# Kernel optimization log

Measured on AMD Instinct MI355X. Metric: run time of the kernel, lower is better.

Reference implementation:

```python
import jax, jax.numpy as jnp
import numpy as np

TEMPERATURE = 10.0
N_CLASSES = 10


def _sqdist(a, b):
    # squared euclidean distances, [Na, Nb] == torch.cdist(a, b) ** 2
    an = jnp.sum(a * a, axis=1)[:, None]
    bn = jnp.sum(b * b, axis=1)[None, :]
    return jnp.maximum(an + bn - 2.0 * (a @ b.T), 0.0)


def setup_inputs() -> dict:
    key = jax.random.key(0)
    ks = jax.random.split(key, 6)
    B, N, D, H, C = 512, 4096, 512, 2048, N_CLASSES
    return {
        "x": jax.random.normal(ks[0], (B, D), dtype=jnp.float32),
        "star_features": jax.random.normal(ks[1], (N, D), dtype=jnp.float32),
        "from_features": jax.random.normal(ks[2], (N, D), dtype=jnp.float32),
        "star_label_ids": jax.random.randint(ks[3], (N,), 0, C),
        "W1": jax.random.normal(ks[4], (D, H), dtype=jnp.float32) * 0.02,
        "b1": jnp.zeros((H,), dtype=jnp.float32),
        "W2": jax.random.normal(ks[5], (H, C), dtype=jnp.float32) * 0.02,
        "b2": jnp.zeros((C,), dtype=jnp.float32),
    }


def _transport_features(x, feats_to, star_feats):
    # dists: [N_star, B]
    d = _sqdist(star_feats, x)
    d = d / jnp.mean(d, axis=0, keepdims=True)
    e = jnp.exp(-TEMPERATURE * d)                    # [N_star, B]
    w = feats_to.T @ e                               # [d_to, B]
    return (w / jnp.sum(e, axis=0, keepdims=True)).T  # [B, d_to]


def reference(x, star_features, from_features, star_label_ids, W1, b1, W2, b2):
    B = x.shape[0]
    C = N_CLASSES
    # --- exact-match lookup against dataset_star features (fused eq+all reduce) ---
    mask = jnp.all(x[:, None, :] == star_features[None, :, :], axis=2)  # [B, N_star]
    matched = jnp.any(mask, axis=1)                                      # [B]
    match_idx = jnp.argmax(mask, axis=1)                                 # [B]
    # --- transport features: matched samples take aligned dataset sample, rest use OT map ---
    xt_unmatched = _transport_features(x, from_features, star_features)  # [B, d]
    xt_matched = from_features[match_idx]                                # [B, d]
    x_transported = jnp.where(matched[:, None], xt_matched, xt_unmatched)
    # --- run the model in the transported domain (MLP classifier) ---
    h = jax.nn.relu(x_transported @ W1 + b1)
    logits = h @ W2 + b2                                                 # [B, C]
    # --- project_labels: preds and one-hot unique labels have equal dim -> cdist/argmin branch ---
    unique_labels = jnp.eye(C, dtype=logits.dtype)
    closest = jnp.argmin(_sqdist(logits, unique_labels), axis=1)
    y_proj = unique_labels[closest]                                      # [B, C] (unused by 'all_features')
    # --- transport_labels, method='all_features': feature-distance-weighted average of star labels ---
    d2 = _sqdist(from_features, x_transported)                           # [N_from, B]
    d2 = d2 / jnp.mean(d2, axis=0, keepdims=True)
    e2 = jnp.exp(-TEMPERATURE * d2)
    star_labels = jax.nn.one_hot(star_label_ids, C, dtype=x.dtype)       # [N_star, C]
    y_star = (star_labels.T @ e2 / jnp.sum(e2, axis=0, keepdims=True)).T  # [B, C]
    # single (model, dataset) pair -> sum/len is identity
    return y_star
```

## Files before the change

### kernel.cpp

```cpp
#include <hip/hip_runtime.h>

#define TEMP 10.0f
#define NS 4096
#define BB 512
#define DDIM 512
#define NCLS 10

typedef short bf16x8 __attribute__((ext_vector_type(8)));
typedef float f32x4 __attribute__((ext_vector_type(4)));

__device__ inline short f2bf(float f) {
    unsigned u = __builtin_bit_cast(unsigned, f);
    u += 0x7FFFu + ((u >> 16) & 1u);
    return (short)(u >> 16);
}
__device__ inline float bf2f(short h) {
    unsigned u = ((unsigned)(unsigned short)h) << 16;
    return __builtin_bit_cast(float, u);
}

__global__ void init_midx(int* midx) {
    int t = blockIdx.x * 256 + threadIdx.x;
    if (t < BB) midx[t] = NS;
}

__global__ __launch_bounds__(256)
void conv512(const float* __restrict__ in, short* __restrict__ outb,
             float* __restrict__ n2) {
    int row = blockIdx.x * 4 + (threadIdx.x >> 6);
    int l = threadIdx.x & 63;
    const float4* p = (const float4*)(in + (size_t)row * DDIM) + l * 2;
    float4 a = p[0], b = p[1];
    float s = a.x*a.x + a.y*a.y + a.z*a.z + a.w*a.w
            + b.x*b.x + b.y*b.y + b.z*b.z + b.w*b.w;
    bf16x8 h;
    h[0]=f2bf(a.x); h[1]=f2bf(a.y); h[2]=f2bf(a.z); h[3]=f2bf(a.w);
    h[4]=f2bf(b.x); h[5]=f2bf(b.y); h[6]=f2bf(b.z); h[7]=f2bf(b.w);
    *(bf16x8*)(outb + (size_t)row * DDIM + l * 8) = h;
    #pragma unroll
    for (int off = 32; off > 0; off >>= 1) s += __shfl_down(s, off);
    if (l == 0) n2[row] = s;
}

__global__ __launch_bounds__(256)
void convT(const float* __restrict__ in, short* __restrict__ outb) {
    __shared__ short tile[64][72];
    int n0 = blockIdx.x * 64, d0 = blockIdx.y * 64;
    int t = threadIdx.x;
    int r = t >> 4, c4 = (t & 15) * 4;
    #pragma unroll
    for (int rr = 0; rr < 64; rr += 16) {
        float4 v = *(const float4*)(in + (size_t)(n0 + r + rr) * DDIM + d0 + c4);
        tile[r + rr][c4 + 0] = f2bf(v.x);
        tile[r + rr][c4 + 1] = f2bf(v.y);
        tile[r + rr][c4 + 2] = f2bf(v.z);
        tile[r + rr][c4 + 3] = f2bf(v.w);
    }
    __syncthreads();
    int dr = t >> 2, nco = (t & 3) * 16;
    short tmp[16];
    #pragma unroll
    for (int q = 0; q < 16; ++q) tmp[q] = tile[nco + q][dr];
    short* op = outb + (size_t)(d0 + dr) * NS + n0 + nco;
    *(bf16x8*)op       = *(bf16x8*)tmp;
    *(bf16x8*)(op + 8) = *(bf16x8*)(tmp + 8);
}

__global__ void match_kernel(const float* __restrict__ x, const float* __restrict__ star,
                             int* __restrict__ midx) {
    int i = blockIdx.x * blockDim.x + threadIdx.x;
    if (i >= NS * BB) return;
    int b = i & (BB - 1);
    int n = i >> 9;
    const float* xr = x + (size_t)b * DDIM;
    const float* sr = star + (size_t)n * DDIM;
    if (xr[0] != sr[0]) return;
    for (int k = 1; k < DDIM; ++k) if (xr[k] != sr[k]) return;
    atomicMin(&midx[b], n);
}

#define BM 64
#define BN 128
#define BK 64
#define LDSP 72
template<int MODE>
__global__ __launch_bounds__(256)
void gemm_bt(const short* __restrict__ A, const short* __restrict__ B, int K,
             int kslab, int nt, const float* __restrict__ an2,
             const float* __restrict__ bn2, float* __restrict__ C, int ldc,
             size_t cstride) {
    __shared__ short As[2][BM][LDSP];
    __shared__ short Bs[2][BN][LDSP];
    int t = threadIdx.x;
    int m0 = blockIdx.x * BM;
    int n0 = blockIdx.y * BN;
    int kbase = blockIdx.z * kslab;
    float* Cp = C + (size_t)blockIdx.z * cstride;
    int wid = t >> 6, lane = t & 63;
    int wr = wid >> 1, wc = wid & 1;
    int lr = lane & 15, lk = lane >> 4;

    int ar = t >> 2, ak = (t & 3) * 16;
    int br = t >> 1, bk = (t & 1) * 32;
    const short* Ag = A + (size_t)(m0 + ar) * K + kbase + ak;
    const short* Bg = B + (size_t)(n0 + br) * K + kbase + bk;

    f32x4 acc[2][4] = {};
    bf16x8 ra0 = *(const bf16x8*)Ag;
    bf16x8 ra1 = *(const bf16x8*)(Ag + 8);
    bf16x8 rb0 = *(const bf16x8*)Bg;
    bf16x8 rb1 = *(const bf16x8*)(Bg + 8);
    bf16x8 rb2 = *(const bf16x8*)(Bg + 16);
    bf16x8 rb3 = *(const bf16x8*)(Bg + 24);
    int cur = 0;
    *(bf16x8*)&As[0][ar][ak]      = ra0;
    *(bf16x8*)&As[0][ar][ak + 8]  = ra1;
    *(bf16x8*)&Bs[0][br][bk]      = rb0;
    *(bf16x8*)&Bs[0][br][bk + 8]  = rb1;
    *(bf16x8*)&Bs[0][br][bk + 16] = rb2;
    *(bf16x8*)&Bs[0][br][bk + 24] = rb3;

    for (int it = 0; it < nt; ++it) {
        __syncthreads();
        if (it + 1 < nt) {
            int ko = (it + 1) * BK;
            ra0 = *(const bf16x8*)(Ag + ko);
            ra1 = *(const bf16x8*)(Ag + ko + 8);
            rb0 = *(const bf16x8*)(Bg + ko);
            rb1 = *(const bf16x8*)(Bg + ko + 8);
            rb2 = *(const bf16x8*)(Bg + ko + 16);
            rb3 = *(const bf16x8*)(Bg + ko + 24);
        }
        #pragma unroll
        for (int ks = 0; ks < 2; ++ks) {
            int k0 = ks * 32 + lk * 8;
            bf16x8 af[2], bfr[4];
            #pragma unroll
            for (int i = 0; i < 2; ++i)
                af[i] = *(const bf16x8*)&As[cur][wr * 32 + i * 16 + lr][k0];
            #pragma unroll
            for (int j = 0; j < 4; ++j)
                bfr[j] = *(const bf16x8*)&Bs[cur][wc * 64 + j * 16 + lr][k0];
            #pragma unroll
            for (int i = 0; i < 2; ++i)
                #pragma unroll
                for (int j = 0; j < 4; ++j)
                    acc[i][j] = __builtin_amdgcn_mfma_f32_16x16x32_bf16(
                        af[i], bfr[j], acc[i][j], 0, 0, 0);
        }
        if (it + 1 < nt) {
            cur ^= 1;
            *(bf16x8*)&As[cur][ar][ak]      = ra0;
            *(bf16x8*)&As[cur][ar][ak + 8]  = ra1;
            *(bf16x8*)&Bs[cur][br][bk]      = rb0;
            *(bf16x8*)&Bs[cur][br][bk + 8]  = rb1;
            *(bf16x8*)&Bs[cur][br][bk + 16] = rb2;
            *(bf16x8*)&Bs[cur][br][bk + 24] = rb3;
        }
    }
    #pragma unroll
    for (int i = 0; i < 2; ++i) {
        #pragma unroll
        for (int r = 0; r < 4; ++r) {
            int gm = m0 + wr * 32 + i * 16 + lk * 4 + r;
            float a2 = (MODE == 1) ? an2[gm] : 0.0f;
            #pragma unroll
            for (int j = 0; j < 4; ++j) {
                int gn = n0 + wc * 64 + j * 16 + lr;
                float v = acc[i][j][r];
                if (MODE == 1) v = fmaxf(a2 + bn2[gn] - 2.0f * v, 0.0f);
                Cp[(size_t)gm * ldc + gn] = v;
            }
        }
    }
}

__device__ inline float block_sum(float s, float* red) {
    #pragma unroll
    for (int off = 32; off > 0; off >>= 1) s += __shfl_down(s, off);
    int wid = threadIdx.x >> 6;
    if ((threadIdx.x & 63) == 0) red[wid] = s;
    __syncthreads();
    float tot = red[0] + red[1] + red[2] + red[3];
    __syncthreads();
    return tot;
}

__global__ __launch_bounds__(256)
void exp_rows(const float* __restrict__ dT, short* __restrict__ eT,
              float* __restrict__ sumE) {
    __shared__ float red[4];
    int b = blockIdx.x;
    int t = threadIdx.x;
    const float* row = dT + (size_t)b * NS;
    float4 v[4];
    float s = 0.f;
    #pragma unroll
    for (int q = 0; q < 4; ++q) {
        v[q] = *(const float4*)(row + t * 16 + q * 4);
        s += v[q].x + v[q].y + v[q].z + v[q].w;
    }
    float tot = block_sum(s, red);
    float scale = -TEMP * (float)NS / tot;
    float se = 0.f;
    bf16x8 h0, h1;
    #pragma unroll
    for (int q = 0; q < 4; ++q) {
        #pragma unroll
        for (int e = 0; e < 4; ++e) {
            float ev = __expf(v[q][e] * scale);
            short hh = f2bf(ev);
            se += bf2f(hh);
            if (q < 2) h0[q * 4 + e] = hh; else h1[(q - 2) * 4 + e] = hh;
        }
    }
    short* op = eT + (size_t)b * NS + t * 16;
    *(bf16x8*)op       = h0;
    *(bf16x8*)(op + 8) = h1;
    float setot = block_sum(se, red);
    if (t == 0) sumE[b] = setot;
}

__global__ __launch_bounds__(256)
void xt_fin(const float* __restrict__ wpart, const float* __restrict__ sumE,
            const int* __restrict__ midx, const float* __restrict__ fromf,
            short* __restrict__ xtb, float* __restrict__ xtn2) {
    __shared__ float red[4];
    int b = blockIdx.x;
    int t = threadIdx.x;
    int d = t * 2;
    int mi = midx[b];
    float inv = 1.0f / sumE[b];
    float v0 = 0.f, v1 = 0.f;
    #pragma unroll
    for (int sl = 0; sl < 8; ++sl) {
        float2 p = *(const float2*)(wpart + (size_t)sl * (BB * DDIM) + (size_t)b * DDIM + d);
        v0 += p.x; v1 += p.y;
    }
    v0 *= inv; v1 *= inv;
    if (mi < NS) {
        v0 = fromf[(size_t)mi * DDIM + d];
        v1 = fromf[(size_t)mi * DDIM + d + 1];
    }
    xtb[(size_t)b * DDIM + d]     = f2bf(v0);
    xtb[(size_t)b * DDIM + d + 1] = f2bf(v1);
    float tot = block_sum(v0 * v0 + v1 * v1, red);
    if (t == 0) xtn2[b] = tot;
}

__global__ __launch_bounds__(256)
void ystar(const float* __restrict__ d2T, const int* __restrict__ labels,
           float* __restrict__ out) {
    __shared__ float red[4];
    __shared__ float cred[NCLS + 1][4];
    int b = blockIdx.x;
    int t = threadIdx.x;
    const float* row = d2T + (size_t)b * NS;
    float4 v[4];
    float s = 0.f;
    #pragma unroll
    for (int q = 0; q < 4; ++q) {
        v[q] = *(const float4*)(row + t * 16 + q * 4);
        s += v[q].x + v[q].y + v[q].z + v[q].w;
    }
    float tot = block_sum(s, red);
    float scale = -TEMP * (float)NS / tot;
    float accs[NCLS] = {};
    float te = 0.f;
    #pragma unroll
    for (int q = 0; q < 4; ++q) {
        int4 lb = *(const int4*)(labels + t * 16 + q * 4);
        int lbl[4] = {lb.x, lb.y, lb.z, lb.w};
        #pragma unroll
        for (int e = 0; e < 4; ++e) {
            float ev = __expf(v[q][e] * scale);
            te += ev;
            #pragma unroll
            for (int c = 0; c < NCLS; ++c) accs[c] += (lbl[e] == c) ? ev : 0.f;
        }
    }
    int wid = t >> 6, lane = t & 63;
    #pragma unroll
    for (int c = 0; c < NCLS + 1; ++c) {
        float sv = (c < NCLS) ? accs[c] : te;
        #pragma unroll
        for (int off = 32; off > 0; off >>= 1) sv += __shfl_down(sv, off);
        if (lane == 0) cred[c][wid] = sv;
    }
    __syncthreads();
    if (t < NCLS) {
        float num = cred[t][0] + cred[t][1] + cred[t][2] + cred[t][3];
        float den = cred[NCLS][0] + cred[NCLS][1] + cred[NCLS][2] + cred[NCLS][3];
        out[b * NCLS + t] = num / den;
    }
}

extern "C" void kernel_launch(void* const* d_in, const int* in_sizes, int n_in,
                              void* d_out, int out_size, void* d_ws, size_t ws_size,
                              hipStream_t stream) {
    const float* x     = (const float*)d_in[0];
    const float* star  = (const float*)d_in[1];
    const float* from  = (const float*)d_in[2];
    const int*   label = (const int*)d_in[3];
    float* out = (float*)d_out;

    float* F    = (float*)d_ws;
    float* Dbuf = F;
    short* Sb   = (short*)(F + 2097152);
    short* Eb   = (short*)(F + 3145728);
    short* Xb   = (short*)(F + 4194304);
    short* XTb  = (short*)(F + 4325376);
    float* sn2  = F + 4456448;
    float* fn2  = sn2 + 4096;
    float* xn2  = fn2 + 4096;
    float* xtn2 = xn2 + 512;
    float* sumE = xtn2 + 512;
    int*   midx = (int*)(sumE + 512);

    init_midx<<<2, 256, 0, stream>>>(midx);
    conv512<<<NS / 4, 256, 0, stream>>>(star, Sb, sn2);
    conv512<<<BB / 4, 256, 0, stream>>>(x, Xb, xn2);
    match_kernel<<<(NS * BB) / 256, 256, 0, stream>>>(x, star, midx);
    gemm_bt<1><<<dim3(BB / BM, NS / BN), 256, 0, stream>>>(
        Xb, Sb, DDIM, DDIM, DDIM / BK, xn2, sn2, Dbuf, NS, 0);
    convT<<<dim3(NS / 64, DDIM / 64), 256, 0, stream>>>(from, Sb);
    exp_rows<<<BB, 256, 0, stream>>>(Dbuf, Eb, sumE);
    gemm_bt<0><<<dim3(BB / BM, DDIM / BN, 8), 256, 0, stream>>>(
        Eb, Sb, NS, NS / 8, (NS / 8) / BK, nullptr, nullptr, Dbuf, DDIM,
        (size_t)BB * DDIM);
    conv512<<<NS / 4, 256, 0, stream>>>(from, Sb, fn2);
    xt_fin<<<BB, 256, 0, stream>>>(Dbuf, sumE, midx, from, XTb, xtn2);
    gemm_bt<1><<<dim3(BB / BM, NS / BN), 256, 0, stream>>>(
        XTb, Sb, DDIM, DDIM, DDIM / BK, xtn2, fn2, Dbuf, NS, 0);
    ystar<<<BB, 256, 0, stream>>>(Dbuf, label, out);
}
```

Baseline: 78.75 us.

## Fuse prep kernels, filter exact-match by first column, shrink GEMM tiles

```diff
diff --git a/kernel.cpp b/kernel.cpp
--- a/kernel.cpp
+++ b/kernel.cpp
@@ -5,6 +5,7 @@
 #define BB 512
 #define DDIM 512
 #define NCLS 10
+#define LDSP 72
 
 typedef short bf16x8 __attribute__((ext_vector_type(8)));
 typedef float f32x4 __attribute__((ext_vector_type(4)));
@@ -19,38 +20,46 @@
     return __builtin_bit_cast(float, u);
 }
 
-__global__ void init_midx(int* midx) {
-    int t = blockIdx.x * 256 + threadIdx.x;
-    if (t < BB) midx[t] = NS;
-}
-
-__global__ __launch_bounds__(256)
-void conv512(const float* __restrict__ in, short* __restrict__ outb,
-             float* __restrict__ n2) {
-    int row = blockIdx.x * 4 + (threadIdx.x >> 6);
-    int l = threadIdx.x & 63;
-    const float4* p = (const float4*)(in + (size_t)row * DDIM) + l * 2;
-    float4 a = p[0], b = p[1];
-    float s = a.x*a.x + a.y*a.y + a.z*a.z + a.w*a.w
-            + b.x*b.x + b.y*b.y + b.z*b.z + b.w*b.w;
-    bf16x8 h;
-    h[0]=f2bf(a.x); h[1]=f2bf(a.y); h[2]=f2bf(a.z); h[3]=f2bf(a.w);
-    h[4]=f2bf(b.x); h[5]=f2bf(b.y); h[6]=f2bf(b.z); h[7]=f2bf(b.w);
-    *(bf16x8*)(outb + (size_t)row * DDIM + l * 8) = h;
-    #pragma unroll
-    for (int off = 32; off > 0; off >>= 1) s += __shfl_down(s, off);
-    if (l == 0) n2[row] = s;
-}
-
-__global__ __launch_bounds__(256)
-void convT(const float* __restrict__ in, short* __restrict__ outb) {
-    __shared__ short tile[64][72];
-    int n0 = blockIdx.x * 64, d0 = blockIdx.y * 64;
-    int t = threadIdx.x;
+__global__ __launch_bounds__(256)
+void prep(const float* __restrict__ x, const float* __restrict__ star,
+          const float* __restrict__ from,
+          short* __restrict__ Xb, short* __restrict__ Sb,
+          short* __restrict__ FTb, short* __restrict__ Fb,
+          float* __restrict__ xn2, float* __restrict__ sn2, float* __restrict__ fn2,
+          float* __restrict__ scol, float* __restrict__ xcol, int* __restrict__ midx)
+{
+    int bid = blockIdx.x, t = threadIdx.x;
+    if (bid < 2176) {
+        const float* in; short* outb; float* n2; float* colb; int rowbase;
+        if (bid < 1024)      { in = star; outb = Sb; n2 = sn2; colb = scol; rowbase = bid * 4; }
+        else if (bid < 1152) { in = x;    outb = Xb; n2 = xn2; colb = xcol; rowbase = (bid - 1024) * 4; }
+        else                 { in = from; outb = Fb; n2 = fn2; colb = nullptr; rowbase = (bid - 1152) * 4; }
+        if (bid == 1024) { midx[t] = NS; midx[256 + t] = NS; }
+        int row = rowbase + (t >> 6);
+        int l = t & 63;
+        const float4* p = (const float4*)(in + (size_t)row * DDIM) + l * 2;
+        float4 a = p[0], b = p[1];
+        float s = a.x*a.x + a.y*a.y + a.z*a.z + a.w*a.w
+                + b.x*b.x + b.y*b.y + b.z*b.z + b.w*b.w;
+        bf16x8 h;
+        h[0]=f2bf(a.x); h[1]=f2bf(a.y); h[2]=f2bf(a.z); h[3]=f2bf(a.w);
+        h[4]=f2bf(b.x); h[5]=f2bf(b.y); h[6]=f2bf(b.z); h[7]=f2bf(b.w);
+        *(bf16x8*)(outb + (size_t)row * DDIM + l * 8) = h;
+        #pragma unroll
+        for (int off = 32; off > 0; off >>= 1) s += __shfl_down(s, off);
+        if (l == 0) {
+            n2[row] = s;
+            if (colb) colb[row] = a.x;
+        }
+        return;
+    }
+    __shared__ short tile[64][LDSP];
+    int tid2 = bid - 2176;
+    int n0 = (tid2 & 63) * 64, d0 = (tid2 >> 6) * 64;
     int r = t >> 4, c4 = (t & 15) * 4;
     #pragma unroll
     for (int rr = 0; rr < 64; rr += 16) {
-        float4 v = *(const float4*)(in + (size_t)(n0 + r + rr) * DDIM + d0 + c4);
+        float4 v = *(const float4*)(from + (size_t)(n0 + r + rr) * DDIM + d0 + c4);
         tile[r + rr][c4 + 0] = f2bf(v.x);
         tile[r + rr][c4 + 1] = f2bf(v.y);
         tile[r + rr][c4 + 2] = f2bf(v.z);
@@ -61,101 +70,107 @@
     short tmp[16];
     #pragma unroll
     for (int q = 0; q < 16; ++q) tmp[q] = tile[nco + q][dr];
-    short* op = outb + (size_t)(d0 + dr) * NS + n0 + nco;
+    short* op = FTb + (size_t)(d0 + dr) * NS + n0 + nco;
     *(bf16x8*)op       = *(bf16x8*)tmp;
     *(bf16x8*)(op + 8) = *(bf16x8*)(tmp + 8);
 }
 
-__global__ void match_kernel(const float* __restrict__ x, const float* __restrict__ star,
-                             int* __restrict__ midx) {
-    int i = blockIdx.x * blockDim.x + threadIdx.x;
-    if (i >= NS * BB) return;
-    int b = i & (BB - 1);
-    int n = i >> 9;
-    const float* xr = x + (size_t)b * DDIM;
-    const float* sr = star + (size_t)n * DDIM;
-    if (xr[0] != sr[0]) return;
-    for (int k = 1; k < DDIM; ++k) if (xr[k] != sr[k]) return;
-    atomicMin(&midx[b], n);
-}
-
-#define BM 64
-#define BN 128
-#define BK 64
-#define LDSP 72
 template<int MODE>
 __global__ __launch_bounds__(256)
 void gemm_bt(const short* __restrict__ A, const short* __restrict__ B, int K,
-             int kslab, int nt, const float* __restrict__ an2,
-             const float* __restrict__ bn2, float* __restrict__ C, int ldc,
-             size_t cstride) {
-    __shared__ short As[2][BM][LDSP];
-    __shared__ short Bs[2][BN][LDSP];
+             int nshift, const float* __restrict__ an2, const float* __restrict__ bn2,
+             float* __restrict__ C, int ldc, size_t cstride, int ngemm,
+             const float* __restrict__ x, const float* __restrict__ star,
+             const float* __restrict__ scol, const float* __restrict__ xcol,
+             int* __restrict__ midx)
+{
+    __shared__ short As[2][64][LDSP];
+    __shared__ short Bs[2][64][LDSP];
+    int gid = blockIdx.x;
     int t = threadIdx.x;
-    int m0 = blockIdx.x * BM;
-    int n0 = blockIdx.y * BN;
-    int kbase = blockIdx.z * kslab;
-    float* Cp = C + (size_t)blockIdx.z * cstride;
+    if (gid >= ngemm) {
+        float* xl = (float*)&As[0][0][0];
+        int mb = gid - ngemm;
+        xl[t] = xcol[t]; xl[256 + t] = xcol[256 + t];
+        __syncthreads();
+        #pragma unroll
+        for (int rep = 0; rep < 2; ++rep) {
+            int n = mb * 512 + rep * 256 + t;
+            float sv = scol[n];
+            for (int b = 0; b < BB; ++b) {
+                if (xl[b] == sv) {
+                    const float* xr = x + (size_t)b * DDIM;
+                    const float* sr = star + (size_t)n * DDIM;
+                    bool eq = true;
+                    for (int k = 0; k < DDIM && eq; k += 4) {
+                        float4 xv = *(const float4*)(xr + k);
+                        float4 s4 = *(const float4*)(sr + k);
+                        eq = (xv.x == s4.x) && (xv.y == s4.y) &&
+                             (xv.z == s4.z) && (xv.w == s4.w);
+                    }
+                    if (eq) atomicMin(&midx[b], n);
+                }
+            }
+        }
+        return;
+    }
+    int m0 = (gid & 7) << 6;
+    int n0 = ((gid >> 3) & ((1 << nshift) - 1)) << 6;
+    int z  = gid >> (3 + nshift);
+    int kbase = z * 512;
+    float* Cp = C + (size_t)z * cstride;
     int wid = t >> 6, lane = t & 63;
     int wr = wid >> 1, wc = wid & 1;
     int lr = lane & 15, lk = lane >> 4;
 
     int ar = t >> 2, ak = (t & 3) * 16;
-    int br = t >> 1, bk = (t & 1) * 32;
     const short* Ag = A + (size_t)(m0 + ar) * K + kbase + ak;
-    const short* Bg = B + (size_t)(n0 + br) * K + kbase + bk;
-
-    f32x4 acc[2][4] = {};
+    const short* Bg = B + (size_t)(n0 + ar) * K + kbase + ak;
+
+    f32x4 acc[2][2] = {};
     bf16x8 ra0 = *(const bf16x8*)Ag;
     bf16x8 ra1 = *(const bf16x8*)(Ag + 8);
     bf16x8 rb0 = *(const bf16x8*)Bg;
     bf16x8 rb1 = *(const bf16x8*)(Bg + 8);
-    bf16x8 rb2 = *(const bf16x8*)(Bg + 16);
-    bf16x8 rb3 = *(const bf16x8*)(Bg + 24);
     int cur = 0;
-    *(bf16x8*)&As[0][ar][ak]      = ra0;
-    *(bf16x8*)&As[0][ar][ak + 8]  = ra1;
-    *(bf16x8*)&Bs[0][br][bk]      = rb0;
-    *(bf16x8*)&Bs[0][br][bk + 8]  = rb1;
-    *(bf16x8*)&Bs[0][br][bk + 16] = rb2;
-    *(bf16x8*)&Bs[0][br][bk + 24] = rb3;
-
-    for (int it = 0; it < nt; ++it) {
+    *(bf16x8*)&As[0][ar][ak]     = ra0;
+    *(bf16x8*)&As[0][ar][ak + 8] = ra1;
+    *(bf16x8*)&Bs[0][ar][ak]     = rb0;
+    *(bf16x8*)&Bs[0][ar][ak + 8] = rb1;
+
+    #pragma unroll
+    for (int it = 0; it < 8; ++it) {
         __syncthreads();
-        if (it + 1 < nt) {
-            int ko = (it + 1) * BK;
+        if (it + 1 < 8) {
+            int ko = (it + 1) * 64;
             ra0 = *(const bf16x8*)(Ag + ko);
             ra1 = *(const bf16x8*)(Ag + ko + 8);
             rb0 = *(const bf16x8*)(Bg + ko);
             rb1 = *(const bf16x8*)(Bg + ko + 8);
-            rb2 = *(const bf16x8*)(Bg + ko + 16);
-            rb3 = *(const bf16x8*)(Bg + ko + 24);
         }
         #pragma unroll
         for (int ks = 0; ks < 2; ++ks) {
             int k0 = ks * 32 + lk * 8;
-            bf16x8 af[2], bfr[4];
+            bf16x8 af[2], bfr[2];
             #pragma unroll
             for (int i = 0; i < 2; ++i)
                 af[i] = *(const bf16x8*)&As[cur][wr * 32 + i * 16 + lr][k0];
             #pragma unroll
-            for (int j = 0; j < 4; ++j)
-                bfr[j] = *(const bf16x8*)&Bs[cur][wc * 64 + j * 16 + lr][k0];
+            for (int j = 0; j < 2; ++j)
+                bfr[j] = *(const bf16x8*)&Bs[cur][wc * 32 + j * 16 + lr][k0];
             #pragma unroll
             for (int i = 0; i < 2; ++i)
                 #pragma unroll
-                for (int j = 0; j < 4; ++j)
+                for (int j = 0; j < 2; ++j)
                     acc[i][j] = __builtin_amdgcn_mfma_f32_16x16x32_bf16(
                         af[i], bfr[j], acc[i][j], 0, 0, 0);
         }
-        if (it + 1 < nt) {
+        if (it + 1 < 8) {
             cur ^= 1;
-            *(bf16x8*)&As[cur][ar][ak]      = ra0;
-            *(bf16x8*)&As[cur][ar][ak + 8]  = ra1;
-            *(bf16x8*)&Bs[cur][br][bk]      = rb0;
-            *(bf16x8*)&Bs[cur][br][bk + 8]  = rb1;
-            *(bf16x8*)&Bs[cur][br][bk + 16] = rb2;
-            *(bf16x8*)&Bs[cur][br][bk + 24] = rb3;
+            *(bf16x8*)&As[cur][ar][ak]     = ra0;
+            *(bf16x8*)&As[cur][ar][ak + 8] = ra1;
+            *(bf16x8*)&Bs[cur][ar][ak]     = rb0;
+            *(bf16x8*)&Bs[cur][ar][ak + 8] = rb1;
         }
     }
     #pragma unroll
@@ -165,8 +180,8 @@
             int gm = m0 + wr * 32 + i * 16 + lk * 4 + r;
             float a2 = (MODE == 1) ? an2[gm] : 0.0f;
             #pragma unroll
-            for (int j = 0; j < 4; ++j) {
-                int gn = n0 + wc * 64 + j * 16 + lr;
+            for (int j = 0; j < 2; ++j) {
+                int gn = n0 + wc * 32 + j * 16 + lr;
                 float v = acc[i][j][r];
                 if (MODE == 1) v = fmaxf(a2 + bn2[gn] - 2.0f * v, 0.0f);
                 Cp[(size_t)gm * ldc + gn] = v;
@@ -304,33 +319,35 @@
     const int*   label = (const int*)d_in[3];
     float* out = (float*)d_out;
 
-    float* F    = (float*)d_ws;
-    float* Dbuf = F;
-    short* Sb   = (short*)(F + 2097152);
-    short* Eb   = (short*)(F + 3145728);
-    short* Xb   = (short*)(F + 4194304);
-    short* XTb  = (short*)(F + 4325376);
-    float* sn2  = F + 4456448;
-    float* fn2  = sn2 + 4096;
-    float* xn2  = fn2 + 4096;
-    float* xtn2 = xn2 + 512;
-    float* sumE = xtn2 + 512;
-    int*   midx = (int*)(sumE + 512);
-
-    init_midx<<<2, 256, 0, stream>>>(midx);
-    conv512<<<NS / 4, 256, 0, stream>>>(star, Sb, sn2);
-    conv512<<<BB / 4, 256, 0, stream>>>(x, Xb, xn2);
-    match_kernel<<<(NS * BB) / 256, 256, 0, stream>>>(x, star, midx);
-    gemm_bt<1><<<dim3(BB / BM, NS / BN), 256, 0, stream>>>(
-        Xb, Sb, DDIM, DDIM, DDIM / BK, xn2, sn2, Dbuf, NS, 0);
-    convT<<<dim3(NS / 64, DDIM / 64), 256, 0, stream>>>(from, Sb);
-    exp_rows<<<BB, 256, 0, stream>>>(Dbuf, Eb, sumE);
-    gemm_bt<0><<<dim3(BB / BM, DDIM / BN, 8), 256, 0, stream>>>(
-        Eb, Sb, NS, NS / 8, (NS / 8) / BK, nullptr, nullptr, Dbuf, DDIM,
-        (size_t)BB * DDIM);
-    conv512<<<NS / 4, 256, 0, stream>>>(from, Sb, fn2);
-    xt_fin<<<BB, 256, 0, stream>>>(Dbuf, sumE, midx, from, XTb, xtn2);
-    gemm_bt<1><<<dim3(BB / BM, NS / BN), 256, 0, stream>>>(
-        XTb, Sb, DDIM, DDIM, DDIM / BK, xtn2, fn2, Dbuf, NS, 0);
-    ystar<<<BB, 256, 0, stream>>>(Dbuf, label, out);
-}
+    float* F = (float*)d_ws;
+    float* dT    = F;
+    float* wpart = F + 2097152;
+    float* d2T   = F + 4194304;
+    short* Sb    = (short*)(F + 6291456);
+    short* FTb   = (short*)(F + 7340032);
+    short* Fb    = (short*)(F + 8388608);
+    short* Eb    = (short*)(F + 9437184);
+    short* Xb    = (short*)(F + 10485760);
+    short* XTb   = (short*)(F + 10616832);
+    float* sn2   = F + 10747904;
+    float* fn2   = F + 10752000;
+    float* xn2   = F + 10756096;
+    float* xtn2  = F + 10756608;
+    float* sumE  = F + 10757120;
+    float* scol  = F + 10757632;
+    float* xcol  = F + 10761728;
+    int*   midx  = (int*)(F + 10762240);
+
+    prep<<<2688, 256, 0, stream>>>(x, star, from, Xb, Sb, FTb, Fb,
+                                   xn2, sn2, fn2, scol, xcol, midx);
+    gemm_bt<1><<<520, 256, 0, stream>>>(Xb, Sb, DDIM, 6, xn2, sn2, dT, NS, 0,
+                                        512, x, star, scol, xcol, midx);
+    exp_rows<<<BB, 256, 0, stream>>>(dT, Eb, sumE);
+    gemm_bt<0><<<512, 256, 0, stream>>>(Eb, FTb, NS, 3, nullptr, nullptr, wpart,
+                                        DDIM, (size_t)BB * DDIM,
+                                        512, nullptr, nullptr, nullptr, nullptr, nullptr);
+    xt_fin<<<BB, 256, 0, stream>>>(wpart, sumE, midx, from, XTb, xtn2);
+    gemm_bt<1><<<512, 256, 0, stream>>>(XTb, Fb, DDIM, 6, xtn2, fn2, d2T, NS, 0,
+                                        512, nullptr, nullptr, nullptr, nullptr, nullptr);
+    ystar<<<BB, 256, 0, stream>>>(d2T, label, out);
+}
```

Result: slower. 108.2 us (+37.4%).
